# Performance work log

Measured on AMD Instinct MI355X. Metric: run time of the kernel, lower is better.

## Reference

```python
import jax, jax.numpy as jnp
import numpy as np

# TT decomposition config (from Eff_TTEmbedding args in source)
P = (216, 216, 216)      # auto-factorized p_shapes for n=10,000,000 (216^3 >= n)
Q = (2, 4, 2)            # tt_q_shapes, prod = 16 = embedding_dim
R = (128, 128)           # tt_ranks
NUM_TABLES = 2
BATCH = 1024
NUM_EMB = 10_000_000


def setup_inputs() -> dict:
    key = jax.random.key(0)
    k0, k1, k2, k3 = jax.random.split(key, 4)
    # sparse indices per TT table: [n_tables, batch]
    lS_i = jax.random.randint(k3, (NUM_TABLES, BATCH), 0, NUM_EMB, dtype=jnp.int64)
    # TT cores, weight_dist='uniform'
    core0 = jax.random.uniform(k0, (NUM_TABLES, P[0], Q[0] * R[0]), dtype=jnp.float32, minval=-0.01, maxval=0.01)
    core1 = jax.random.uniform(k1, (NUM_TABLES, P[1], R[0] * Q[1] * R[1]), dtype=jnp.float32, minval=-0.01, maxval=0.01)
    core2 = jax.random.uniform(k2, (NUM_TABLES, P[2], R[1] * Q[2]), dtype=jnp.float32, minval=-0.01, maxval=0.01)
    return {"lS_i": lS_i, "core0": core0, "core1": core1, "core2": core2}


def _tt_lookup(idx, c0, c1, c2):
    """TT embedding lookup for one table. idx: [B] int; returns [B, prod(Q)]."""
    B = idx.shape[0]
    # mixed-radix decomposition of flat index into (i0, i1, i2)
    i0 = idx // (P[1] * P[2])
    i1 = (idx // P[2]) % P[1]
    i2 = idx % P[2]
    # gather TT core slices (the memory-bound irregular access)
    A = c0[i0].reshape(B, Q[0], R[0])            # [B, 2, 128]
    Bm = c1[i1].reshape(B, R[0], Q[1] * R[1])    # [B, 128, 512]
    C = c2[i2].reshape(B, R[1], Q[2])            # [B, 128, 2]
    # chained small matmuls along TT ranks
    AB = jnp.einsum('bqr,brs->bqs', A, Bm).reshape(B, Q[0] * Q[1], R[1])  # [B, 8, 128]
    out = jnp.einsum('bqr,brs->bqs', AB, C)      # [B, 8, 2]
    return out.reshape(B, Q[0] * Q[1] * Q[2])    # [B, 16]


def reference(lS_i, core0, core1, core2):
    # per-table dispatch (forward returns one embedding bag per TT table)
    return jax.vmap(_tt_lookup)(lS_i, core0, core1, core2)  # [n_tables, B, 16]
```

## Files before the change

kernel.cpp:

```cpp
#include <hip/hip_runtime.h>


#define LOOKUPS 2048
#define C1_ROW  65536
#define ROW_F4  128

__global__ __launch_bounds__(256) void tt_lookup_kernel(
    const int* __restrict__ idx32,
    const float* __restrict__ c0,
    const float* __restrict__ c1,
    const float* __restrict__ c2,
    float* __restrict__ out)
{
    __shared__ float lds_a[2][256];

    const int half = threadIdx.x >> 7;
    const int tl   = threadIdx.x & 127;
    const int g    = blockIdx.x * 2 + half;
    const int table = g >> 10;

    const bool is64 = (idx32[1] == 0) & (idx32[3] == 0) &
                      (idx32[5] == 0) & (idx32[7] == 0);
    const unsigned int idx = is64
        ? (unsigned int)((const long long*)idx32)[g]
        : (unsigned int)idx32[g];

    const unsigned int i0  = idx / 46656u;
    const unsigned int rem = idx - i0 * 46656u;
    const unsigned int i1  = rem / 216u;
    const unsigned int i2  = rem - i1 * 216u;

    const float* arow = c0 + ((size_t)table * 216 + i0) * 256;
    const float* brow = c1 + ((size_t)table * 216 + i1) * C1_ROW;
    const float* crow = c2 + ((size_t)table * 216 + i2) * 256;

    lds_a[half][tl]       = arow[tl];
    lds_a[half][tl + 128] = arow[tl + 128];
    __syncthreads();

    float4 acc0 = {0.f, 0.f, 0.f, 0.f};
    float4 acc1 = {0.f, 0.f, 0.f, 0.f};
    const float4* b4 = (const float4*)brow + tl;
#pragma unroll 8
    for (int r = 0; r < 128; ++r) {
        const float4 bv = b4[r * ROW_F4];
        const float a0 = lds_a[half][r];
        const float a1 = lds_a[half][128 + r];
        acc0.x += a0 * bv.x; acc0.y += a0 * bv.y;
        acc0.z += a0 * bv.z; acc0.w += a0 * bv.w;
        acc1.x += a1 * bv.x; acc1.y += a1 * bv.y;
        acc1.z += a1 * bv.z; acc1.w += a1 * bv.w;
    }

    const int q1 = tl >> 5;
    const int r1 = (tl & 31) * 4;
    const float4 cA = *(const float4*)(crow + r1 * 2);
    const float4 cB = *(const float4*)(crow + r1 * 2 + 4);

    float p00 = acc0.x*cA.x + acc0.y*cA.z + acc0.z*cB.x + acc0.w*cB.z;
    float p01 = acc0.x*cA.y + acc0.y*cA.w + acc0.z*cB.y + acc0.w*cB.w;
    float p10 = acc1.x*cA.x + acc1.y*cA.z + acc1.z*cB.x + acc1.w*cB.z;
    float p11 = acc1.x*cA.y + acc1.y*cA.w + acc1.z*cB.y + acc1.w*cB.w;

#pragma unroll
    for (int m = 16; m >= 1; m >>= 1) {
        p00 += __shfl_xor(p00, m);
        p01 += __shfl_xor(p01, m);
        p10 += __shfl_xor(p10, m);
        p11 += __shfl_xor(p11, m);
    }

    if ((tl & 31) == 0) {
        float* o = out + (size_t)g * 16;
        o[q1 * 2 + 0]     = p00;
        o[q1 * 2 + 1]     = p01;
        o[8 + q1 * 2 + 0] = p10;
        o[8 + q1 * 2 + 1] = p11;
    }
}

extern "C" void kernel_launch(void* const* d_in, const int* in_sizes, int n_in,
                              void* d_out, int out_size, void* d_ws, size_t ws_size,
                              hipStream_t stream) {
    const int*   idx = (const int*)d_in[0];
    const float* c0  = (const float*)d_in[1];
    const float* c1  = (const float*)d_in[2];
    const float* c2  = (const float*)d_in[3];
    float* out = (float*)d_out;
    tt_lookup_kernel<<<dim3(LOOKUPS / 2), dim3(256), 0, stream>>>(idx, c0, c1, c2, out);
}
```

Baseline: 190.0 us.

## Group lookups by middle TT core row to reuse core1 slice loads

A new single-block prep kernel buckets the 2048 lookups by (table, i1) with an LDS counting sort and writes offsets, counts and packed i0/i2 to workspace. The main kernel launches one block per (table, i1) group and column half, streams the 256 KB core1 slice once, and multiplies it against up to eight gathered core0 rows at a time. This is meant to cut the redundant core1 traffic when several lookups share an i1. It adds an extra serial launch, heavy register use for 8x2 float4 accumulators, and load imbalance across groups.

```diff
diff --git a/kernel.cpp b/kernel.cpp
--- a/kernel.cpp
+++ b/kernel.cpp
@@ -1,81 +1,164 @@
 #include <hip/hip_runtime.h>
 
 
-#define LOOKUPS 2048
-#define C1_ROW  65536
-#define ROW_F4  128
+#define NGROUPS 432
+#define NLOOK   2048
 
-__global__ __launch_bounds__(256) void tt_lookup_kernel(
-    const int* __restrict__ idx32,
+__global__ __launch_bounds__(512) void tt_prep(const int* __restrict__ idx32,
+                                               int* __restrict__ w) {
+    __shared__ int cnt[NGROUPS];
+    __shared__ int scan[512];
+    __shared__ int cursor[NGROUPS];
+    const int tid = threadIdx.x;
+
+    for (int i = tid; i < NGROUPS; i += 512) cnt[i] = 0;
+    __syncthreads();
+
+    const bool is64 = (idx32[1] == 0) & (idx32[3] == 0) &
+                      (idx32[5] == 0) & (idx32[7] == 0);
+
+    int grp[4];
+#pragma unroll
+    for (int j = 0; j < 4; ++j) {
+        const int id = tid + j * 512;
+        const unsigned idx = is64 ? (unsigned)((const long long*)idx32)[id]
+                                  : (unsigned)idx32[id];
+        const unsigned i0  = idx / 46656u;
+        const unsigned rem = idx - i0 * 46656u;
+        const unsigned i1  = rem / 216u;
+        const unsigned i2  = rem - i1 * 216u;
+        const int table = id >> 10;
+        grp[j] = table * 216 + (int)i1;
+        w[2912 + id] = (int)((i0 << 16) | i2);
+        atomicAdd(&cnt[grp[j]], 1);
+    }
+    __syncthreads();
+
+    scan[tid] = (tid < NGROUPS) ? cnt[tid] : 0;
+    __syncthreads();
+    for (int off = 1; off < 512; off <<= 1) {
+        const int v   = scan[tid];
+        const int add = (tid >= off) ? scan[tid - off] : 0;
+        __syncthreads();
+        scan[tid] = v + add;
+        __syncthreads();
+    }
+    if (tid < NGROUPS) {
+        const int st = scan[tid] - cnt[tid];
+        w[tid]        = st;
+        w[432 + tid]  = cnt[tid];
+        cursor[tid]   = st;
+    }
+    __syncthreads();
+
+#pragma unroll
+    for (int j = 0; j < 4; ++j) {
+        const int id  = tid + j * 512;
+        const int pos = atomicAdd(&cursor[grp[j]], 1);
+        w[864 + pos] = id;
+    }
+}
+
+__global__ __launch_bounds__(64) void tt_main(
     const float* __restrict__ c0,
     const float* __restrict__ c1,
     const float* __restrict__ c2,
+    const int* __restrict__ w,
     float* __restrict__ out)
 {
-    __shared__ float lds_a[2][256];
+    const int g = blockIdx.x;
+    const int h = blockIdx.y;
+    const int m = w[432 + g];
+    if (m == 0) return;
+    const int s0    = w[g];
+    const int table = g / 216;
+    const int i1    = g - table * 216;
+    const int tl    = threadIdx.x;
 
-    const int half = threadIdx.x >> 7;
-    const int tl   = threadIdx.x & 127;
-    const int g    = blockIdx.x * 2 + half;
-    const int table = g >> 10;
+    const float4* b4 = (const float4*)(c1 + (((size_t)table * 216 + i1) << 16))
+                       + (h * 64 + tl);
 
-    const bool is64 = (idx32[1] == 0) & (idx32[3] == 0) &
-                      (idx32[5] == 0) & (idx32[7] == 0);
-    const unsigned int idx = is64
-        ? (unsigned int)((const long long*)idx32)[g]
-        : (unsigned int)idx32[g];
+    __shared__ float A[8][256];
+    __shared__ int   s_id[8];
+    __shared__ int   s_aux[8];
 
-    const unsigned int i0  = idx / 46656u;
-    const unsigned int rem = idx - i0 * 46656u;
-    const unsigned int i1  = rem / 216u;
-    const unsigned int i2  = rem - i1 * 216u;
-
-    const float* arow = c0 + ((size_t)table * 216 + i0) * 256;
-    const float* brow = c1 + ((size_t)table * 216 + i1) * C1_ROW;
-    const float* crow = c2 + ((size_t)table * 216 + i2) * 256;
-
-    lds_a[half][tl]       = arow[tl];
-    lds_a[half][tl + 128] = arow[tl + 128];
-    __syncthreads();
-
-    float4 acc0 = {0.f, 0.f, 0.f, 0.f};
-    float4 acc1 = {0.f, 0.f, 0.f, 0.f};
-    const float4* b4 = (const float4*)brow + tl;
-#pragma unroll 8
-    for (int r = 0; r < 128; ++r) {
-        const float4 bv = b4[r * ROW_F4];
-        const float a0 = lds_a[half][r];
-        const float a1 = lds_a[half][128 + r];
-        acc0.x += a0 * bv.x; acc0.y += a0 * bv.y;
-        acc0.z += a0 * bv.z; acc0.w += a0 * bv.w;
-        acc1.x += a1 * bv.x; acc1.y += a1 * bv.y;
-        acc1.z += a1 * bv.z; acc1.w += a1 * bv.w;
-    }
-
-    const int q1 = tl >> 5;
-    const int r1 = (tl & 31) * 4;
-    const float4 cA = *(const float4*)(crow + r1 * 2);
-    const float4 cB = *(const float4*)(crow + r1 * 2 + 4);
-
-    float p00 = acc0.x*cA.x + acc0.y*cA.z + acc0.z*cB.x + acc0.w*cB.z;
-    float p01 = acc0.x*cA.y + acc0.y*cA.w + acc0.z*cB.y + acc0.w*cB.w;
-    float p10 = acc1.x*cA.x + acc1.y*cA.z + acc1.z*cB.x + acc1.w*cB.z;
-    float p11 = acc1.x*cA.y + acc1.y*cA.w + acc1.z*cB.y + acc1.w*cB.w;
+    for (int base = 0; base < m; base += 8) {
+        const int cl = min(8, m - base);
+        __syncthreads();
+        if (tl < 8) {
+            const bool ok = tl < cl;
+            const int id  = ok ? w[864 + s0 + base + tl] : 0;
+            s_id[tl]  = id;
+            s_aux[tl] = ok ? w[2912 + id] : -1;
+        }
+        __syncthreads();
 
 #pragma unroll
-    for (int m = 16; m >= 1; m >>= 1) {
-        p00 += __shfl_xor(p00, m);
-        p01 += __shfl_xor(p01, m);
-        p10 += __shfl_xor(p10, m);
-        p11 += __shfl_xor(p11, m);
-    }
+        for (int l = 0; l < 8; ++l) {
+            const int aux = s_aux[l];
+            if (aux >= 0) {
+                const float* ar = c0 + ((size_t)table * 216 + (aux >> 16)) * 256;
+#pragma unroll
+                for (int k = 0; k < 4; ++k) {
+                    const int e = tl + 64 * k;
+                    A[l][e] = ar[((e & 1) << 7) + (e >> 1)];
+                }
+            } else {
+#pragma unroll
+                for (int k = 0; k < 4; ++k) A[l][tl + 64 * k] = 0.f;
+            }
+        }
+        __syncthreads();
 
-    if ((tl & 31) == 0) {
-        float* o = out + (size_t)g * 16;
-        o[q1 * 2 + 0]     = p00;
-        o[q1 * 2 + 1]     = p01;
-        o[8 + q1 * 2 + 0] = p10;
-        o[8 + q1 * 2 + 1] = p11;
+        float4 acc[8][2];
+#pragma unroll
+        for (int l = 0; l < 8; ++l) {
+            acc[l][0] = make_float4(0.f, 0.f, 0.f, 0.f);
+            acc[l][1] = make_float4(0.f, 0.f, 0.f, 0.f);
+        }
+
+#pragma unroll 8
+        for (int r = 0; r < 128; ++r) {
+            const float4 bv = b4[(size_t)r * 128];
+#pragma unroll
+            for (int l = 0; l < 8; ++l) {
+                const float2 av = ((const float2*)A[l])[r];
+                acc[l][0].x += av.x * bv.x; acc[l][0].y += av.x * bv.y;
+                acc[l][0].z += av.x * bv.z; acc[l][0].w += av.x * bv.w;
+                acc[l][1].x += av.y * bv.x; acc[l][1].y += av.y * bv.y;
+                acc[l][1].z += av.y * bv.z; acc[l][1].w += av.y * bv.w;
+            }
+        }
+
+        const int q1 = 2 * h + (tl >> 5);
+        const int r1 = (tl & 31) * 4;
+#pragma unroll
+        for (int l = 0; l < 8; ++l) {
+            if (l < cl) {
+                const int aux = s_aux[l];
+                const float* crow = c2 + ((size_t)table * 216 + (aux & 0xffff)) * 256;
+                const float4 cA = *(const float4*)(crow + r1 * 2);
+                const float4 cB = *(const float4*)(crow + r1 * 2 + 4);
+                float p00 = acc[l][0].x*cA.x + acc[l][0].y*cA.z + acc[l][0].z*cB.x + acc[l][0].w*cB.z;
+                float p01 = acc[l][0].x*cA.y + acc[l][0].y*cA.w + acc[l][0].z*cB.y + acc[l][0].w*cB.w;
+                float p10 = acc[l][1].x*cA.x + acc[l][1].y*cA.z + acc[l][1].z*cB.x + acc[l][1].w*cB.z;
+                float p11 = acc[l][1].x*cA.y + acc[l][1].y*cA.w + acc[l][1].z*cB.y + acc[l][1].w*cB.w;
+#pragma unroll
+                for (int mm = 16; mm >= 1; mm >>= 1) {
+                    p00 += __shfl_xor(p00, mm);
+                    p01 += __shfl_xor(p01, mm);
+                    p10 += __shfl_xor(p10, mm);
+                    p11 += __shfl_xor(p11, mm);
+                }
+                if ((tl & 31) == 0) {
+                    float* o = out + (size_t)s_id[l] * 16;
+                    o[q1 * 2 + 0]     = p00;
+                    o[q1 * 2 + 1]     = p01;
+                    o[8 + q1 * 2 + 0] = p10;
+                    o[8 + q1 * 2 + 1] = p11;
+                }
+            }
+        }
     }
 }
 
@@ -87,5 +170,8 @@
     const float* c1  = (const float*)d_in[2];
     const float* c2  = (const float*)d_in[3];
     float* out = (float*)d_out;
-    tt_lookup_kernel<<<dim3(LOOKUPS / 2), dim3(256), 0, stream>>>(idx, c0, c1, c2, out);
+    int* w = (int*)d_ws;
+
+    tt_prep<<<dim3(1), dim3(512), 0, stream>>>(idx, w);
+    tt_main<<<dim3(NGROUPS, 2), dim3(64), 0, stream>>>(c0, c1, c2, w, out);
 }
```

Result: slower. 241.6 us (+27.2%).
